# Performance work log

Measured on AMD Instinct MI355X. Metric: run time of the kernel, lower is better.

The kernel has to match this reference:

```python
import jax, jax.numpy as jnp
import numpy as np

RATES = (6, 12, 18, 24)  # dilation/padding per branch


def _offset_conv(x, w, b, rate):
    # mmcv ConvModule with norm_cfg=None: conv (bias=True) + ReLU
    y = jax.lax.conv_general_dilated(
        x, w, window_strides=(1, 1),
        padding=[(rate, rate), (rate, rate)],
        rhs_dilation=(rate, rate),
        dimension_numbers=('NCHW', 'OIHW', 'NCHW'))
    return jax.nn.relu(y + b[None, :, None, None])


def _deform_conv(x, offset, w, rate):
    # DCNv1: 3x3 deformable conv, stride 1, padding=dilation=rate,
    # deformable_groups=1, no bias. Zero padding outside image (bilinear).
    B, C, H, W = x.shape
    K = 9  # 3x3 kernel taps, row-major; offset channels [2k]=dy, [2k+1]=dx
    ky = (jnp.arange(K) // 3 - 1).astype(x.dtype)
    kx = (jnp.arange(K) % 3 - 1).astype(x.dtype)
    off = offset.reshape(B, K, 2, H, W)
    gy = jnp.arange(H, dtype=x.dtype)
    gx = jnp.arange(W, dtype=x.dtype)
    # sampling coords [B,K,H,W]: p0 + dilated kernel offset + learned offset
    py = gy[None, None, :, None] + ky[None, :, None, None] * rate + off[:, :, 0]
    px = gx[None, None, None, :] + kx[None, :, None, None] * rate + off[:, :, 1]
    y0 = jnp.floor(py)
    x0 = jnp.floor(px)
    wy = (py - y0)[:, None]  # [B,1,K,H,W]
    wx = (px - x0)[:, None]
    y0i = y0.astype(jnp.int32)
    x0i = x0.astype(jnp.int32)
    xf = x.reshape(B, C, H * W)

    def gather(yi, xi):
        valid = (yi >= 0) & (yi < H) & (xi >= 0) & (xi < W)
        idx = (jnp.clip(yi, 0, H - 1) * W + jnp.clip(xi, 0, W - 1)).reshape(B, K * H * W)
        v = jnp.take_along_axis(xf, idx[:, None, :], axis=2).reshape(B, C, K, H, W)
        return v * valid[:, None].astype(x.dtype)

    samp = (gather(y0i, x0i) * (1 - wy) * (1 - wx)
            + gather(y0i, x0i + 1) * (1 - wy) * wx
            + gather(y0i + 1, x0i) * wy * (1 - wx)
            + gather(y0i + 1, x0i + 1) * wy * wx)  # [B,C,K,H,W]
    return jnp.einsum('oik,bikhw->bohw', w.reshape(w.shape[0], C, K), samp)


def setup_inputs() -> dict:
    key = jax.random.key(0)
    k1, k2, k3 = jax.random.split(key, 3)
    B, C, H, W = 2, 256, 64, 64
    Cout, R = 256, len(RATES)
    x = jax.random.normal(k1, (B, C, H, W), dtype=jnp.float32)
    dweights = jax.random.normal(k2, (R, Cout, C, 3, 3), dtype=jnp.float32) * 0.02
    oweights = jax.random.normal(k3, (R, 18, C, 3, 3), dtype=jnp.float32) * 0.01
    obias = jnp.zeros((R, 18), dtype=jnp.float32)
    return {"x": x, "dweights": dweights, "oweights": oweights, "obias": obias}


def reference(x, dweights, oweights, obias):
    R = len(RATES)
    outs = []
    for i in range(R):
        j = (i - 1) % R  # source quirk: offsets[i-1] (wraps to last for i=0)
        off = _offset_conv(x, oweights[j], obias[j], RATES[j])
        outs.append(_deform_conv(x, off, dweights[i], RATES[i]))
    return jnp.concatenate(outs, axis=1)
```

## Files before the change

### kernel.cpp

```cpp
#include <hip/hip_runtime.h>
#include <hip/hip_bf16.h>

typedef __attribute__((ext_vector_type(4))) float f32x4;
typedef __attribute__((ext_vector_type(2))) _Float16 h2;
typedef __attribute__((ext_vector_type(8))) _Float16 f16x8;

#define LGKM_BARRIER() asm volatile("s_waitcnt lgkmcnt(0)\n\ts_barrier" ::: "memory")

__global__ __launch_bounds__(256) void transpose_x_hwc_f16(const float* __restrict__ x,
                                                           unsigned short* __restrict__ x16h) {
    __shared__ float s[64][65];
    int blk = blockIdx.x;
    int b = blk >> 8, ct = (blk >> 6) & 3, pt = blk & 63;
    int c0 = ct * 64, p0 = pt * 64;
    int tid = threadIdx.x;
    int tr = tid >> 6, tc = tid & 63;
#pragma unroll
    for (int i = 0; i < 16; ++i) {
        int c = i * 4 + tr;
        s[c][tc] = x[((size_t)b * 256 + c0 + c) * 4096 + p0 + tc];
    }
    __syncthreads();
#pragma unroll
    for (int i = 0; i < 16; ++i) {
        int pp = i * 4 + tr;
        _Float16 h = (_Float16)s[tc][pp];
        x16h[((size_t)b * 4096 + p0 + pp) * 256 + c0 + tc] = *(unsigned short*)&h;
    }
}

__global__ __launch_bounds__(256) void transpose_dw_f16(const float* __restrict__ dw,
                                                        unsigned short* __restrict__ wTh) {
    int idx = blockIdx.x * 256 + threadIdx.x;
    int c = idx & 255;
    int o = (idx >> 8) & 255;
    int rest = idx >> 16;
    int k = rest % 9, i = rest / 9;
    _Float16 h = (_Float16)dw[(((i << 8) + o) * 256 + c) * 9 + k];
    wTh[idx] = *(unsigned short*)&h;
}

__global__ __launch_bounds__(256) void transpose_ow_f16(const float* __restrict__ ow,
                                                        unsigned short* __restrict__ owTh) {
    int idx = blockIdx.x * 256 + threadIdx.x;
    int c = idx & 255;
    int m = (idx >> 8) & 31;
    int rk = idx >> 13;
    int k = rk % 9, r = rk / 9;
    float v = (m < 18) ? ow[((r * 18 + m) * 256 + c) * 9 + k] : 0.f;
    _Float16 h = (_Float16)v;
    owTh[idx] = *(unsigned short*)&h;
}

__global__ __launch_bounds__(512) void offset_mfma2f(const unsigned short* __restrict__ x16h,
                                                     const unsigned short* __restrict__ owTh,
                                                     const float* __restrict__ obias,
                                                     float* __restrict__ off) {
    __shared__ short    s_a[4][32][8];
    __shared__ short    s_b[4][128][8];
    __shared__ int      s_pix[9][128];
    __shared__ unsigned s_msk[9][128];

    const int blk = blockIdx.x;
    const int r = (blk & 7) >> 1, b = blk & 1;
    const int px0 = (blk >> 3) << 7;
    const int rate = 6 * (r + 1);

    const int tid = threadIdx.x;
    const int lane = tid & 63;
    const int w = tid >> 6;
    const int kg = lane >> 4, lm = lane & 15;
    const int sg = tid >> 7, spx = tid & 127;
    const int mA = (tid & 127) >> 2, kgA = tid & 3;

    const unsigned short* xbh = x16h + (size_t)b * 1048576;
    const unsigned short* wrb = owTh + (size_t)r * 9 * 32 * 256;

    for (int e = tid; e < 1152; e += 512) {
        int k = e >> 7, pl = e & 127;
        int pg = px0 + pl;
        int yy = (pg >> 6) + (k / 3 - 1) * rate;
        int xx = (pg & 63) + (k % 3 - 1) * rate;
        bool v = ((unsigned)yy < 64u) && ((unsigned)xx < 64u);
        int cy = min(max(yy, 0), 63), cx = min(max(xx, 0), 63);
        s_pix[k][pl] = cy * 64 + cx;
        s_msk[k][pl] = v ? 0xFFFFFFFFu : 0u;
    }
    __syncthreads();

    f32x4 acc0 = (f32x4)(0.f), acc1 = (f32x4)(0.f);

    uint4 a, v;
    if (tid < 128) a = *(const uint4*)(wrb + (size_t)mA * 256 + kgA * 8);
    {
        int pix = s_pix[0][spx];
        v = *(const uint4*)(xbh + (size_t)pix * 256 + sg * 8);
    }
    unsigned m = s_msk[0][spx];

    for (int t = 0; t < 72; ++t) {
        uint4 pk = make_uint4(v.x & m, v.y & m, v.z & m, v.w & m);

        LGKM_BARRIER();
        if (tid < 128) *(uint4*)&s_a[kgA][mA][0] = a;
        *(uint4*)&s_b[sg][spx][0] = pk;
        LGKM_BARRIER();

        if (t < 71) {
            int tn = t + 1, tapn = tn >> 3, c0n = (tn & 7) << 5;
            if (tid < 128)
                a = *(const uint4*)(wrb + ((size_t)tapn * 32 + mA) * 256 + c0n + kgA * 8);
            int pix = s_pix[tapn][spx];
            m = s_msk[tapn][spx];
            v = *(const uint4*)(xbh + (size_t)pix * 256 + c0n + sg * 8);
        }

        f16x8 bf  = *(const f16x8*)&s_b[kg][w * 16 + lm][0];
        f16x8 af0 = *(const f16x8*)&s_a[kg][lm][0];
        f16x8 af1 = *(const f16x8*)&s_a[kg][16 + lm][0];
        acc0 = __builtin_amdgcn_mfma_f32_16x16x32_f16(af0, bf, acc0, 0, 0, 0);
        acc1 = __builtin_amdgcn_mfma_f32_16x16x32_f16(af1, bf, acc1, 0, 0, 0);
    }

    const float* bias = obias + r * 18;
    float* ob = off + (size_t)(r * 2 + b) * 18 * 4096;
    int px = px0 + w * 16 + lm;
#pragma unroll
    for (int reg = 0; reg < 4; ++reg) {
        int mm = kg * 4 + reg;
        ob[(size_t)mm * 4096 + px] = fmaxf(acc0[reg] + bias[mm], 0.f);
        int m1 = 16 + mm;
        if (m1 < 18)
            ob[(size_t)m1 * 4096 + px] = fmaxf(acc1[reg] + bias[m1], 0.f);
    }
}

__global__ __launch_bounds__(512, 2) void deform_mfma9(const unsigned short* __restrict__ x16h,
                                                       const unsigned short* __restrict__ wTh,
                                                       const float* __restrict__ off,
                                                       float* __restrict__ out) {
    __shared__ short  s_a[256][64];
    __shared__ short  s_b[64][64];
    __shared__ int4   s_pix[9][64];
    __shared__ float4 s_wt[9][64];

    const int blk = blockIdx.x;
    const int i = (blk & 7) >> 1, b = blk & 1;
    const int px0 = (blk >> 3) << 6;
    const int r = (i + 3) & 3;
    const int rate = 6 * (i + 1);

    const int tid = threadIdx.x;
    const int lane = tid & 63;
    const int w = tid >> 6;
    const int wo = w >> 1, wp = w & 1;
    const int kg = lane >> 4, lm = lane & 15;
    const int pxS = tid >> 3, chgS = tid & 7;
    const int oA = tid >> 3, partA = tid & 7;
    const int colA = (partA * 8) ^ ((oA & 7) * 8);

    const unsigned short* xbh = x16h + (size_t)b * 1048576;
    const float* offb = off + (size_t)(r * 2 + b) * 18 * 4096;
    const unsigned short* wib = wTh + (size_t)i * 9 * 65536;

    for (int e = tid; e < 576; e += 512) {
        int k = e >> 6, pl = e & 63;
        int pg = px0 + pl;
        int yy = pg >> 6, xc = pg & 63;
        float dy = offb[(size_t)(2 * k) * 4096 + pg];
        float dx = offb[(size_t)(2 * k + 1) * 4096 + pg];
        float py = (float)(yy + (k / 3 - 1) * rate) + dy;
        float pxf = (float)(xc + (k % 3 - 1) * rate) + dx;
        float fy = floorf(py), fx = floorf(pxf);
        int y0 = (int)fy, x0 = (int)fx;
        float wy = py - fy, wx = pxf - fx;
        float vy0 = ((unsigned)y0 < 64u) ? 1.f : 0.f;
        float vy1 = ((unsigned)(y0 + 1) < 64u) ? 1.f : 0.f;
        float vx0 = ((unsigned)x0 < 64u) ? 1.f : 0.f;
        float vx1 = ((unsigned)(x0 + 1) < 64u) ? 1.f : 0.f;
        int cy0 = min(max(y0, 0), 63), cy1 = min(max(y0 + 1, 0), 63);
        int cx0 = min(max(x0, 0), 63), cx1 = min(max(x0 + 1, 0), 63);
        s_pix[k][pl] = make_int4(cy0 * 64 + cx0, cy0 * 64 + cx1,
                                 cy1 * 64 + cx0, cy1 * 64 + cx1);
        s_wt[k][pl] = make_float4(vy0 * vx0 * (1.f - wy) * (1.f - wx),
                                  vy0 * vx1 * (1.f - wy) * wx,
                                  vy1 * vx0 * wy * (1.f - wx),
                                  vy1 * vx1 * wy * wx);
    }
    __syncthreads();

    f32x4 acc[4][2];
#pragma unroll
    for (int mi = 0; mi < 4; ++mi) {
        acc[mi][0] = (f32x4)(0.f);
        acc[mi][1] = (f32x4)(0.f);
    }

    uint4 a0, a1, a2, a3, v0, v1, v2, v3;
    {
        const unsigned short* wrow = wib + partA * 8;
        a0 = *(const uint4*)(wrow + (size_t)(oA      ) * 256);
        a1 = *(const uint4*)(wrow + (size_t)(oA +  64) * 256);
        a2 = *(const uint4*)(wrow + (size_t)(oA + 128) * 256);
        a3 = *(const uint4*)(wrow + (size_t)(oA + 192) * 256);
        int4 p = s_pix[0][pxS];
        const unsigned short* xch = xbh + chgS * 8;
        v0 = *(const uint4*)(xch + ((size_t)p.x << 8));
        v1 = *(const uint4*)(xch + ((size_t)p.y << 8));
        v2 = *(const uint4*)(xch + ((size_t)p.z << 8));
        v3 = *(const uint4*)(xch + ((size_t)p.w << 8));
    }

    for (int t = 0; t < 36; ++t) {
        const int tap = t >> 2;

        uint4 pk;
        {
            float4 qwf = s_wt[tap][pxS];
            h2 qx = (h2)((_Float16)qwf.x), qy = (h2)((_Float16)qwf.y);
            h2 qz = (h2)((_Float16)qwf.z), qv = (h2)((_Float16)qwf.w);
            h2 r0 = (*(h2*)&v0.x) * qx + (*(h2*)&v1.x) * qy + (*(h2*)&v2.x) * qz + (*(h2*)&v3.x) * qv;
            h2 r1 = (*(h2*)&v0.y) * qx + (*(h2*)&v1.y) * qy + (*(h2*)&v2.y) * qz + (*(h2*)&v3.y) * qv;
            h2 r2 = (*(h2*)&v0.z) * qx + (*(h2*)&v1.z) * qy + (*(h2*)&v2.z) * qz + (*(h2*)&v3.z) * qv;
            h2 r3 = (*(h2*)&v0.w) * qx + (*(h2*)&v1.w) * qy + (*(h2*)&v2.w) * qz + (*(h2*)&v3.w) * qv;
            pk = make_uint4(*(unsigned*)&r0, *(unsigned*)&r1, *(unsigned*)&r2, *(unsigned*)&r3);
        }

        LGKM_BARRIER();
        *(uint4*)&s_a[oA      ][colA] = a0;
        *(uint4*)&s_a[oA +  64][colA] = a1;
        *(uint4*)&s_a[oA + 128][colA] = a2;
        *(uint4*)&s_a[oA + 192][colA] = a3;
        *(uint4*)&s_b[pxS][(chgS ^ (pxS & 7)) * 8] = pk;
        LGKM_BARRIER();

        if (t < 35) {
            int tn = t + 1, tapn = tn >> 2, c0n = (tn & 3) << 6;
            const unsigned short* wrow = wib + (size_t)tapn * 65536 + c0n + partA * 8;
            a0 = *(const uint4*)(wrow + (size_t)(oA      ) * 256);
            a1 = *(const uint4*)(wrow + (size_t)(oA +  64) * 256);
            a2 = *(const uint4*)(wrow + (size_t)(oA + 128) * 256);
            a3 = *(const uint4*)(wrow + (size_t)(oA + 192) * 256);
            int4 p = s_pix[tapn][pxS];
            const unsigned short* xch = xbh + c0n + chgS * 8;
            v0 = *(const uint4*)(xch + ((size_t)p.x << 8));
            v1 = *(const uint4*)(xch + ((size_t)p.y << 8));
            v2 = *(const uint4*)(xch + ((size_t)p.z << 8));
            v3 = *(const uint4*)(xch + ((size_t)p.w << 8));
        }

#pragma unroll
        for (int kf = 0; kf < 2; ++kf) {
            int oct = kf * 4 + kg;
            int bcol = (oct ^ (lm & 7)) * 8;
            f16x8 bf0 = *(const f16x8*)&s_b[wp * 32 + lm][bcol];
            f16x8 bf1 = *(const f16x8*)&s_b[wp * 32 + 16 + lm][bcol];
#pragma unroll
            for (int mi = 0; mi < 4; ++mi) {
                int o = wo * 64 + mi * 16 + lm;
                int col = (oct * 8) ^ ((o & 7) * 8);
                f16x8 af = *(const f16x8*)&s_a[o][col];
                acc[mi][0] = __builtin_amdgcn_mfma_f32_16x16x32_f16(af, bf0, acc[mi][0], 0, 0, 0);
                acc[mi][1] = __builtin_amdgcn_mfma_f32_16x16x32_f16(af, bf1, acc[mi][1], 0, 0, 0);
            }
        }
    }

    float* ob = out + ((size_t)b * 1024 + i * 256) * 4096;
#pragma unroll
    for (int mi = 0; mi < 4; ++mi) {
        int o = wo * 64 + mi * 16 + kg * 4;
#pragma unroll
        for (int ni = 0; ni < 2; ++ni) {
            int pg = px0 + wp * 32 + ni * 16 + lm;
#pragma unroll
            for (int reg = 0; reg < 4; ++reg)
                ob[(size_t)(o + reg) * 4096 + pg] = acc[mi][ni][reg];
        }
    }
}

extern "C" void kernel_launch(void* const* d_in, const int* in_sizes, int n_in,
                              void* d_out, int out_size, void* d_ws, size_t ws_size,
                              hipStream_t stream) {
    const float* x  = (const float*)d_in[0];
    const float* dw = (const float*)d_in[1];
    const float* ow = (const float*)d_in[2];
    const float* ob = (const float*)d_in[3];
    float* out = (float*)d_out;

    float* ws  = (float*)d_ws;
    float* off = ws;
    unsigned short* wTh  = (unsigned short*)(ws + 589824);
    unsigned short* owTh = wTh + 2359296;
    unsigned short* x16h = (unsigned short*)(ws + 1916928);

    transpose_x_hwc_f16<<<512, 256, 0, stream>>>(x, x16h);
    transpose_dw_f16<<<9216, 256, 0, stream>>>(dw, wTh);
    transpose_ow_f16<<<1152, 256, 0, stream>>>(ow, owTh);
    offset_mfma2f<<<256, 512, 0, stream>>>(x16h, owTh, ob, off);
    deform_mfma9<<<512, 512, 0, stream>>>(x16h, wTh, off, out);
}
```

Before: 113.4 us.

## Double-buffer deform LDS tiles, widen offset K-step, and tile weight transpose

The deform kernel now uses two LDS buffers for weights and sampled values. Staging the next step overlaps the MFMA work on the current one, so each iteration needs one barrier instead of two. The offset conv kernel handles 64 channels per iteration instead of 32, which halves the loop trips and barriers. The deform-weight transpose now reads contiguous rows through shared memory, one block per output channel, instead of making strided scalar reads. Double buffering doubles LDS use, which at 2 blocks per CU could cut occupancy and adds register pressure.

```diff
diff --git a/kernel.cpp b/kernel.cpp
--- a/kernel.cpp
+++ b/kernel.cpp
@@ -6,6 +6,15 @@
 typedef __attribute__((ext_vector_type(8))) _Float16 f16x8;
 
 #define LGKM_BARRIER() asm volatile("s_waitcnt lgkmcnt(0)\n\ts_barrier" ::: "memory")
+
+__device__ __forceinline__ uint4 lerp4(uint4 c0, uint4 c1, uint4 c2, uint4 c3,
+                                       h2 qx, h2 qy, h2 qz, h2 qv) {
+    h2 r0 = (*(h2*)&c0.x) * qx + (*(h2*)&c1.x) * qy + (*(h2*)&c2.x) * qz + (*(h2*)&c3.x) * qv;
+    h2 r1 = (*(h2*)&c0.y) * qx + (*(h2*)&c1.y) * qy + (*(h2*)&c2.y) * qz + (*(h2*)&c3.y) * qv;
+    h2 r2 = (*(h2*)&c0.z) * qx + (*(h2*)&c1.z) * qy + (*(h2*)&c2.z) * qz + (*(h2*)&c3.z) * qv;
+    h2 r3 = (*(h2*)&c0.w) * qx + (*(h2*)&c1.w) * qy + (*(h2*)&c2.w) * qz + (*(h2*)&c3.w) * qv;
+    return make_uint4(*(unsigned*)&r0, *(unsigned*)&r1, *(unsigned*)&r2, *(unsigned*)&r3);
+}
 
 __global__ __launch_bounds__(256) void transpose_x_hwc_f16(const float* __restrict__ x,
                                                            unsigned short* __restrict__ x16h) {
@@ -31,13 +40,20 @@
 
 __global__ __launch_bounds__(256) void transpose_dw_f16(const float* __restrict__ dw,
                                                         unsigned short* __restrict__ wTh) {
-    int idx = blockIdx.x * 256 + threadIdx.x;
-    int c = idx & 255;
-    int o = (idx >> 8) & 255;
-    int rest = idx >> 16;
-    int k = rest % 9, i = rest / 9;
-    _Float16 h = (_Float16)dw[(((i << 8) + o) * 256 + c) * 9 + k];
-    wTh[idx] = *(unsigned short*)&h;
+    __shared__ float s[2304];
+    int blk = blockIdx.x;
+    int i = blk >> 8, o = blk & 255;
+    const float* src = dw + (size_t)(i * 256 + o) * 2304;
+    int tid = threadIdx.x;
+#pragma unroll
+    for (int e = tid; e < 576; e += 256)
+        *(float4*)&s[e * 4] = *(const float4*)&src[e * 4];
+    __syncthreads();
+#pragma unroll
+    for (int k = 0; k < 9; ++k) {
+        _Float16 h = (_Float16)s[tid * 9 + k];
+        wTh[(((size_t)i * 9 + k) * 256 + o) * 256 + tid] = *(unsigned short*)&h;
+    }
 }
 
 __global__ __launch_bounds__(256) void transpose_ow_f16(const float* __restrict__ ow,
@@ -52,12 +68,12 @@
     owTh[idx] = *(unsigned short*)&h;
 }
 
-__global__ __launch_bounds__(512) void offset_mfma2f(const unsigned short* __restrict__ x16h,
+__global__ __launch_bounds__(512) void offset_mfma3f(const unsigned short* __restrict__ x16h,
                                                      const unsigned short* __restrict__ owTh,
                                                      const float* __restrict__ obias,
                                                      float* __restrict__ off) {
-    __shared__ short    s_a[4][32][8];
-    __shared__ short    s_b[4][128][8];
+    __shared__ short    s_a[8][32][8];
+    __shared__ short    s_b[8][128][8];
     __shared__ int      s_pix[9][128];
     __shared__ unsigned s_msk[9][128];
 
@@ -90,36 +106,52 @@
 
     f32x4 acc0 = (f32x4)(0.f), acc1 = (f32x4)(0.f);
 
-    uint4 a, v;
-    if (tid < 128) a = *(const uint4*)(wrb + (size_t)mA * 256 + kgA * 8);
+    uint4 a_lo, a_hi, v_lo, v_hi;
+    if (tid < 128) {
+        a_lo = *(const uint4*)(wrb + (size_t)mA * 256 + kgA * 8);
+        a_hi = *(const uint4*)(wrb + (size_t)mA * 256 + 32 + kgA * 8);
+    }
     {
         int pix = s_pix[0][spx];
-        v = *(const uint4*)(xbh + (size_t)pix * 256 + sg * 8);
+        v_lo = *(const uint4*)(xbh + (size_t)pix * 256 + sg * 8);
+        v_hi = *(const uint4*)(xbh + (size_t)pix * 256 + 32 + sg * 8);
     }
     unsigned m = s_msk[0][spx];
 
-    for (int t = 0; t < 72; ++t) {
-        uint4 pk = make_uint4(v.x & m, v.y & m, v.z & m, v.w & m);
+    for (int t = 0; t < 36; ++t) {
+        uint4 pkl = make_uint4(v_lo.x & m, v_lo.y & m, v_lo.z & m, v_lo.w & m);
+        uint4 pkh = make_uint4(v_hi.x & m, v_hi.y & m, v_hi.z & m, v_hi.w & m);
 
         LGKM_BARRIER();
-        if (tid < 128) *(uint4*)&s_a[kgA][mA][0] = a;
-        *(uint4*)&s_b[sg][spx][0] = pk;
+        if (tid < 128) {
+            *(uint4*)&s_a[kgA][mA][0]     = a_lo;
+            *(uint4*)&s_a[kgA + 4][mA][0] = a_hi;
+        }
+        *(uint4*)&s_b[sg][spx][0]     = pkl;
+        *(uint4*)&s_b[sg + 4][spx][0] = pkh;
         LGKM_BARRIER();
 
-        if (t < 71) {
-            int tn = t + 1, tapn = tn >> 3, c0n = (tn & 7) << 5;
-            if (tid < 128)
-                a = *(const uint4*)(wrb + ((size_t)tapn * 32 + mA) * 256 + c0n + kgA * 8);
+        if (t < 35) {
+            int tn = t + 1, tapn = tn >> 2, c0n = (tn & 3) << 6;
+            if (tid < 128) {
+                a_lo = *(const uint4*)(wrb + ((size_t)tapn * 32 + mA) * 256 + c0n + kgA * 8);
+                a_hi = *(const uint4*)(wrb + ((size_t)tapn * 32 + mA) * 256 + c0n + 32 + kgA * 8);
+            }
             int pix = s_pix[tapn][spx];
             m = s_msk[tapn][spx];
-            v = *(const uint4*)(xbh + (size_t)pix * 256 + c0n + sg * 8);
-        }
-
-        f16x8 bf  = *(const f16x8*)&s_b[kg][w * 16 + lm][0];
-        f16x8 af0 = *(const f16x8*)&s_a[kg][lm][0];
-        f16x8 af1 = *(const f16x8*)&s_a[kg][16 + lm][0];
-        acc0 = __builtin_amdgcn_mfma_f32_16x16x32_f16(af0, bf, acc0, 0, 0, 0);
-        acc1 = __builtin_amdgcn_mfma_f32_16x16x32_f16(af1, bf, acc1, 0, 0, 0);
+            v_lo = *(const uint4*)(xbh + (size_t)pix * 256 + c0n + sg * 8);
+            v_hi = *(const uint4*)(xbh + (size_t)pix * 256 + c0n + 32 + sg * 8);
+        }
+
+#pragma unroll
+        for (int kf = 0; kf < 2; ++kf) {
+            int oct = kf * 4 + kg;
+            f16x8 bf  = *(const f16x8*)&s_b[oct][w * 16 + lm][0];
+            f16x8 af0 = *(const f16x8*)&s_a[oct][lm][0];
+            f16x8 af1 = *(const f16x8*)&s_a[oct][16 + lm][0];
+            acc0 = __builtin_amdgcn_mfma_f32_16x16x32_f16(af0, bf, acc0, 0, 0, 0);
+            acc1 = __builtin_amdgcn_mfma_f32_16x16x32_f16(af1, bf, acc1, 0, 0, 0);
+        }
     }
 
     const float* bias = obias + r * 18;
@@ -135,12 +167,12 @@
     }
 }
 
-__global__ __launch_bounds__(512, 2) void deform_mfma9(const unsigned short* __restrict__ x16h,
-                                                       const unsigned short* __restrict__ wTh,
-                                                       const float* __restrict__ off,
-                                                       float* __restrict__ out) {
-    __shared__ short  s_a[256][64];
-    __shared__ short  s_b[64][64];
+__global__ __launch_bounds__(512, 2) void deform_mfma12(const unsigned short* __restrict__ x16h,
+                                                        const unsigned short* __restrict__ wTh,
+                                                        const float* __restrict__ off,
+                                                        float* __restrict__ out) {
+    __shared__ short  s_a[2][256][64];
+    __shared__ short  s_b[2][64][64];
     __shared__ int4   s_pix[9][64];
     __shared__ float4 s_wt[9][64];
 
@@ -157,7 +189,7 @@
     const int kg = lane >> 4, lm = lane & 15;
     const int pxS = tid >> 3, chgS = tid & 7;
     const int oA = tid >> 3, partA = tid & 7;
-    const int colA = (partA * 8) ^ ((oA & 7) * 8);
+    const int colA = (partA ^ (oA & 7)) * 8;
 
     const unsigned short* xbh = x16h + (size_t)b * 1048576;
     const float* offb = off + (size_t)(r * 2 + b) * 18 * 4096;
@@ -197,73 +229,63 @@
     }
 
     uint4 a0, a1, a2, a3, v0, v1, v2, v3;
-    {
-        const unsigned short* wrow = wib + partA * 8;
+
+    auto load_step = [&](int t) {
+        int tap = t >> 2, c0 = (t & 3) << 6;
+        const unsigned short* wrow = wib + (size_t)tap * 65536 + c0 + partA * 8;
         a0 = *(const uint4*)(wrow + (size_t)(oA      ) * 256);
         a1 = *(const uint4*)(wrow + (size_t)(oA +  64) * 256);
         a2 = *(const uint4*)(wrow + (size_t)(oA + 128) * 256);
         a3 = *(const uint4*)(wrow + (size_t)(oA + 192) * 256);
-        int4 p = s_pix[0][pxS];
-        const unsigned short* xch = xbh + chgS * 8;
+        int4 p = s_pix[tap][pxS];
+        const unsigned short* xch = xbh + c0 + chgS * 8;
         v0 = *(const uint4*)(xch + ((size_t)p.x << 8));
         v1 = *(const uint4*)(xch + ((size_t)p.y << 8));
         v2 = *(const uint4*)(xch + ((size_t)p.z << 8));
         v3 = *(const uint4*)(xch + ((size_t)p.w << 8));
-    }
+    };
+
+    auto stage_step = [&](int t, int buf) {
+        int tap = t >> 2;
+        float4 qwf = s_wt[tap][pxS];
+        h2 qx = (h2)((_Float16)qwf.x), qy = (h2)((_Float16)qwf.y);
+        h2 qz = (h2)((_Float16)qwf.z), qv = (h2)((_Float16)qwf.w);
+        uint4 pk = lerp4(v0, v1, v2, v3, qx, qy, qz, qv);
+        *(uint4*)&s_a[buf][oA      ][colA] = a0;
+        *(uint4*)&s_a[buf][oA +  64][colA] = a1;
+        *(uint4*)&s_a[buf][oA + 128][colA] = a2;
+        *(uint4*)&s_a[buf][oA + 192][colA] = a3;
+        *(uint4*)&s_b[buf][pxS][(chgS ^ (pxS & 7)) * 8] = pk;
+    };
+
+    load_step(0);
+    stage_step(0, 0);
+    load_step(1);
+    LGKM_BARRIER();
 
     for (int t = 0; t < 36; ++t) {
-        const int tap = t >> 2;
-
-        uint4 pk;
-        {
-            float4 qwf = s_wt[tap][pxS];
-            h2 qx = (h2)((_Float16)qwf.x), qy = (h2)((_Float16)qwf.y);
-            h2 qz = (h2)((_Float16)qwf.z), qv = (h2)((_Float16)qwf.w);
-            h2 r0 = (*(h2*)&v0.x) * qx + (*(h2*)&v1.x) * qy + (*(h2*)&v2.x) * qz + (*(h2*)&v3.x) * qv;
-            h2 r1 = (*(h2*)&v0.y) * qx + (*(h2*)&v1.y) * qy + (*(h2*)&v2.y) * qz + (*(h2*)&v3.y) * qv;
-            h2 r2 = (*(h2*)&v0.z) * qx + (*(h2*)&v1.z) * qy + (*(h2*)&v2.z) * qz + (*(h2*)&v3.z) * qv;
-            h2 r3 = (*(h2*)&v0.w) * qx + (*(h2*)&v1.w) * qy + (*(h2*)&v2.w) * qz + (*(h2*)&v3.w) * qv;
-            pk = make_uint4(*(unsigned*)&r0, *(unsigned*)&r1, *(unsigned*)&r2, *(unsigned*)&r3);
-        }
-
-        LGKM_BARRIER();
-        *(uint4*)&s_a[oA      ][colA] = a0;
-        *(uint4*)&s_a[oA +  64][colA] = a1;
-        *(uint4*)&s_a[oA + 128][colA] = a2;
-        *(uint4*)&s_a[oA + 192][colA] = a3;
-        *(uint4*)&s_b[pxS][(chgS ^ (pxS & 7)) * 8] = pk;
-        LGKM_BARRIER();
-
-        if (t < 35) {
-            int tn = t + 1, tapn = tn >> 2, c0n = (tn & 3) << 6;
-            const unsigned short* wrow = wib + (size_t)tapn * 65536 + c0n + partA * 8;
-            a0 = *(const uint4*)(wrow + (size_t)(oA      ) * 256);
-            a1 = *(const uint4*)(wrow + (size_t)(oA +  64) * 256);
-            a2 = *(const uint4*)(wrow + (size_t)(oA + 128) * 256);
-            a3 = *(const uint4*)(wrow + (size_t)(oA + 192) * 256);
-            int4 p = s_pix[tapn][pxS];
-            const unsigned short* xch = xbh + c0n + chgS * 8;
-            v0 = *(const uint4*)(xch + ((size_t)p.x << 8));
-            v1 = *(const uint4*)(xch + ((size_t)p.y << 8));
-            v2 = *(const uint4*)(xch + ((size_t)p.z << 8));
-            v3 = *(const uint4*)(xch + ((size_t)p.w << 8));
-        }
+        const int rb = t & 1;
+
+        if (t < 35) stage_step(t + 1, rb ^ 1);
+        if (t < 34) load_step(t + 2);
 
 #pragma unroll
         for (int kf = 0; kf < 2; ++kf) {
             int oct = kf * 4 + kg;
             int bcol = (oct ^ (lm & 7)) * 8;
-            f16x8 bf0 = *(const f16x8*)&s_b[wp * 32 + lm][bcol];
-            f16x8 bf1 = *(const f16x8*)&s_b[wp * 32 + 16 + lm][bcol];
+            f16x8 bf0 = *(const f16x8*)&s_b[rb][wp * 32 + lm][bcol];
+            f16x8 bf1 = *(const f16x8*)&s_b[rb][wp * 32 + 16 + lm][bcol];
 #pragma unroll
             for (int mi = 0; mi < 4; ++mi) {
                 int o = wo * 64 + mi * 16 + lm;
-                int col = (oct * 8) ^ ((o & 7) * 8);
-                f16x8 af = *(const f16x8*)&s_a[o][col];
+                int col = (oct ^ (o & 7)) * 8;
+                f16x8 af = *(const f16x8*)&s_a[rb][o][col];
                 acc[mi][0] = __builtin_amdgcn_mfma_f32_16x16x32_f16(af, bf0, acc[mi][0], 0, 0, 0);
                 acc[mi][1] = __builtin_amdgcn_mfma_f32_16x16x32_f16(af, bf1, acc[mi][1], 0, 0, 0);
             }
         }
+
+        LGKM_BARRIER();
     }
 
     float* ob = out + ((size_t)b * 1024 + i * 256) * 4096;
@@ -296,8 +318,8 @@
     unsigned short* x16h = (unsigned short*)(ws + 1916928);
 
     transpose_x_hwc_f16<<<512, 256, 0, stream>>>(x, x16h);
-    transpose_dw_f16<<<9216, 256, 0, stream>>>(dw, wTh);
+    transpose_dw_f16<<<1024, 256, 0, stream>>>(dw, wTh);
     transpose_ow_f16<<<1152, 256, 0, stream>>>(ow, owTh);
-    offset_mfma2f<<<256, 512, 0, stream>>>(x16h, owTh, ob, off);
-    deform_mfma9<<<512, 512, 0, stream>>>(x16h, wTh, off, out);
-}
+    offset_mfma3f<<<256, 512, 0, stream>>>(x16h, owTh, ob, off);
+    deform_mfma12<<<512, 512, 0, stream>>>(x16h, wTh, off, out);
+}
```

After: 112.0 us. About the same (-1.3%).
